# Optimization experiments

Measured on AMD Instinct MI355X. Metric: run time of the kernel, lower is better.

Reference implementation:

```python
import jax, jax.numpy as jnp
import numpy as np

B, I, C, H, W = 8, 16, 256, 64, 64  # batch, instances, channels(=in=out), spatial


def setup_inputs() -> dict:
    key = jax.random.key(0)
    ks = jax.random.split(key, 8)
    x = jax.random.normal(ks[0], (B, C, H, W), dtype=jnp.float32)
    masks = jax.random.uniform(ks[1], (B, I, H, W), dtype=jnp.float32)
    # conv_feat: 1x1 conv C->C  -> weight [C_out, C_in]
    Wf = jax.random.normal(ks[2], (C, C), dtype=jnp.float32) * 0.02
    bf = jax.random.normal(ks[3], (C,), dtype=jnp.float32) * 0.02
    # conv_mask: grouped 1x1 conv, groups=I, each 1 -> C channels -> weight [I, C]
    Wm = jax.random.normal(ks[4], (I, C), dtype=jnp.float32) * 0.02
    bm = jax.random.normal(ks[5], (I, C), dtype=jnp.float32) * 0.02
    # conv_out: 1x1 conv C->C
    Wo = jax.random.normal(ks[6], (C, C), dtype=jnp.float32) * 0.02
    bo = jax.random.normal(ks[7], (C,), dtype=jnp.float32) * 0.02
    gamma = jnp.float32(0.5)  # torch init is 0.0; use nonzero so baseline is nontrivial
    return {"x": x, "masks": masks, "Wf": Wf, "bf": bf, "Wm": Wm, "bm": bm,
            "Wo": Wo, "bo": bo, "gamma": gamma}


def reference(x, masks, Wf, bf, Wm, bm, Wo, bo, gamma):
    b, i, h, w = masks.shape
    c = Wf.shape[0]
    # conv_feat: 1x1 conv == per-pixel matmul
    feat = jnp.einsum('bchw,oc->bohw', x, Wf) + bf[:, None, None]  # [B,C,H,W]
    # grouped 1x1 conv_mask: instance i channel -> C channels
    mc = (masks[:, :, None, :, :] * Wm[None, :, :, None, None]
          + bm[None, :, :, None, None])                              # [B,I,C,H,W]
    # softmax over (C*H*W) per instance, as in masks.view(B, I, -1)
    mc = jax.nn.softmax(mc.reshape(b, i, -1), axis=-1).reshape(b, i, c, h, w)
    # loop sum_i conv_out(feat * mask_i)  ==  conv_out_W @ (feat * sum_i mask_i) + I*bias
    msum = mc.sum(axis=1)                                            # [B,C,H,W]
    out = jnp.einsum('bchw,oc->bohw', feat * msum, Wo) + (i * bo)[:, None, None]
    return gamma * out + x
```

## Files before the change

kernel.cpp:

```cpp
#include <hip/hip_runtime.h>


#define NB 8
#define NI 16
#define NC 256
#define HWSZ 4096
#define PT 32

typedef __attribute__((ext_vector_type(8))) short short8;
typedef __attribute__((ext_vector_type(4))) short short4v;
typedef __attribute__((ext_vector_type(4))) float f32x4;

static __device__ inline short f2bf(float f) {
    unsigned u = __builtin_bit_cast(unsigned, f);
    u += 0x7fffu + ((u >> 16) & 1u);
    return (short)(u >> 16);
}
static __device__ inline float bf2f(short h) {
    unsigned u = ((unsigned)(unsigned short)h) << 16;
    return __builtin_bit_cast(float, u);
}


__global__ __launch_bounds__(256)
void setup_kernel(const float* __restrict__ masks, const float* __restrict__ Wm,
                  const float* __restrict__ bm, const float* __restrict__ Wf,
                  const float* __restrict__ Wo, short* __restrict__ AhatF,
                  short* __restrict__ WfF, short* __restrict__ WoF) {
    const int blk = blockIdx.x, t = threadIdx.x;
    if (blk >= NB * NI) {
        const int pid = (blk - NB * NI) * 256 + t;
        const float* src = (pid < 8192) ? Wf : Wo;
        short* dst       = (pid < 8192) ? WfF : WoF;
        const int r  = pid & 8191;
        const int l  = r & 63;
        const int ot = (r >> 6) & 3;
        const int ks = (r >> 8) & 7;
        const int w  = (r >> 11) & 3;
        const int o  = w * 64 + ot * 16 + (l & 15);
        const int c0 = ks * 32 + (l >> 4) * 8;
        float4 v0 = *(const float4*)(src + o * NC + c0);
        float4 v1 = *(const float4*)(src + o * NC + c0 + 4);
        short8 p = { f2bf(v0.x), f2bf(v0.y), f2bf(v0.z), f2bf(v0.w),
                     f2bf(v1.x), f2bf(v1.y), f2bf(v1.z), f2bf(v1.w) };
        *(short8*)(dst + r * 8) = p;
        return;
    }
    const int bi = blk;
    const int b  = bi >> 4;
    const int i  = bi & (NI - 1);
    const float* m = masks + (size_t)bi * HWSZ;

    float s1 = 0.f, s2 = 0.f, s3 = 0.f, s4 = 0.f, s5 = 0.f, s6 = 0.f;
    for (int e = t; e < HWSZ; e += 256) {
        float v = m[e];
        float v2 = v * v, v3 = v2 * v;
        s1 += v; s2 += v2; s3 += v3;
        s4 += v2 * v2; s5 += v2 * v3; s6 += v3 * v3;
    }
    __shared__ float red[7][4];
    float sv[6] = { s1, s2, s3, s4, s5, s6 };
#pragma unroll
    for (int k = 0; k < 6; ++k) {
        float v = sv[k];
#pragma unroll
        for (int off = 32; off > 0; off >>= 1) v += __shfl_down(v, off, 64);
        if ((t & 63) == 0) red[k][t >> 6] = v;
    }
    __syncthreads();
    const float S1 = red[0][0] + red[0][1] + red[0][2] + red[0][3];
    const float S2 = red[1][0] + red[1][1] + red[1][2] + red[1][3];
    const float S3 = red[2][0] + red[2][1] + red[2][2] + red[2][3];
    const float S4 = red[3][0] + red[3][1] + red[3][2] + red[3][3];
    const float S5 = red[4][0] + red[4][1] + red[4][2] + red[4][3];
    const float S6 = red[5][0] + red[5][1] + red[5][2] + red[5][3];

    const int c = t;
    const float w  = Wm[i * NC + c];
    const float eb = __expf(bm[i * NC + c]);
    const float poly = (float)HWSZ
        + w * (S1 + w * (0.5f * S2 + w * ((1.f / 6.f) * S3
        + w * ((1.f / 24.f) * S4 + w * ((1.f / 120.f) * S5
        + w * ((1.f / 720.f) * S6))))));
    float v = eb * poly;
#pragma unroll
    for (int off = 32; off > 0; off >>= 1) v += __shfl_down(v, off, 64);
    if ((t & 63) == 0) red[6][t >> 6] = v;
    __syncthreads();
    const float Z = red[6][0] + red[6][1] + red[6][2] + red[6][3];
    const float a = eb / Z;
    const int wv   = c >> 6;
    const int ot   = (c >> 4) & 3;
    const int ln15 = c & 15;
    const int ks   = i >> 3;
    const int qq   = (i >> 1) & 3;
    const int l    = qq * 16 + ln15;
    const int js   = (i & 1) * 4;
    short4v av = { f2bf(a), f2bf(a * w), f2bf(a * w * w * 0.5f),
                   f2bf(a * w * w * w * (1.f / 6.f)) };
    *(short4v*)(AhatF + ((((b * 4 + wv) * 2 + ks) * 4 + ot) * 64 + l) * 8 + js) = av;
}

__global__ __launch_bounds__(256, 4)
void main_kernel(const float* __restrict__ x, const float* __restrict__ masks,
                 const float* __restrict__ bf_, const float* __restrict__ bo,
                 const float* __restrict__ gamma_p,
                 const short* __restrict__ WfF, const short* __restrict__ WoF,
                 const short* __restrict__ AhatF, float* __restrict__ out) {
    const int blk  = blockIdx.x;
    const int b    = blk >> 7;
    const int hw0  = (blk & 127) << 5;
    const int t    = threadIdx.x;
    const int lane = t & 63;
    const int ln15 = lane & 15;
    const int q    = lane >> 4;
    const int w    = t >> 6;
    const int wo0  = w << 6;

    __shared__ __align__(16) short smem[10752];
    short* sA = smem;
    short* sM = smem + 8448;

    const float* xbase = x + ((size_t)b * NC) * HWSZ + hw0;

    const int cth = t >> 3;
    const int qf  = t & 7;
    float4 xr[8];
#pragma unroll
    for (int it = 0; it < 8; ++it)
        xr[it] = *(const float4*)(xbase + (size_t)(it * 32 + cth) * HWSZ + qf * 4);

    {
        const int i  = t >> 4;
        const int p2 = (t & 15) * 2;
        const float* mp = masks + ((size_t)(b * NI + i)) * HWSZ + hw0 + p2;
        float m0 = mp[0], m1 = mp[1];
        float m0s = m0 * m0, m1s = m1 * m1;
        short4v v0 = { (short)0x3F80, f2bf(m0), f2bf(m0s), f2bf(m0s * m0) };
        short4v v1 = { (short)0x3F80, f2bf(m1), f2bf(m1s), f2bf(m1s * m1) };
        *(short4v*)(sM + p2 * 72 + i * 4) = v0;
        *(short4v*)(sM + (p2 + 1) * 72 + i * 4) = v1;
    }

#pragma unroll
    for (int it = 0; it < 8; ++it) {
        const int c = it * 32 + cth;
        sA[(qf * 4 + 0) * 264 + c] = f2bf(xr[it].x);
        sA[(qf * 4 + 1) * 264 + c] = f2bf(xr[it].y);
        sA[(qf * 4 + 2) * 264 + c] = f2bf(xr[it].z);
        sA[(qf * 4 + 3) * 264 + c] = f2bf(xr[it].w);
    }
    __syncthreads();

    f32x4 feat[4][2];
#pragma unroll
    for (int ot = 0; ot < 4; ++ot)
#pragma unroll
        for (int pt = 0; pt < 2; ++pt) feat[ot][pt] = (f32x4)0.f;
#pragma unroll 4
    for (int ks = 0; ks < 8; ++ks) {
        short8 af[4], bfr[2];
#pragma unroll
        for (int ot = 0; ot < 4; ++ot)
            af[ot] = *(const short8*)(WfF + (((w * 8 + ks) * 4 + ot) * 64 + lane) * 8);
#pragma unroll
        for (int pt = 0; pt < 2; ++pt)
            bfr[pt] = *(const short8*)(sA + (pt * 16 + ln15) * 264 + ks * 32 + q * 8);
#pragma unroll
        for (int ot = 0; ot < 4; ++ot)
#pragma unroll
            for (int pt = 0; pt < 2; ++pt)
                feat[ot][pt] = __builtin_amdgcn_mfma_f32_16x16x32_bf16(
                    af[ot], bfr[pt], feat[ot][pt], 0, 0, 0);
    }
    __syncthreads();

    {
        short8 mfr[2][2];
#pragma unroll
        for (int ks = 0; ks < 2; ++ks)
#pragma unroll
            for (int pt = 0; pt < 2; ++pt)
                mfr[ks][pt] = *(const short8*)(sM + (pt * 16 + ln15) * 72
                                               + ks * 32 + q * 8);
        const short* Ab = AhatF + (size_t)b * 2048 * 8;
#pragma unroll
        for (int ot = 0; ot < 4; ++ot) {
            f32x4 macc[2];
            macc[0] = (f32x4)0.f; macc[1] = (f32x4)0.f;
#pragma unroll
            for (int ks = 0; ks < 2; ++ks) {
                short8 a0 = *(const short8*)(Ab + (((w * 2 + ks) * 4 + ot) * 64
                                                   + lane) * 8);
#pragma unroll
                for (int pt = 0; pt < 2; ++pt)
                    macc[pt] = __builtin_amdgcn_mfma_f32_16x16x32_bf16(
                        a0, mfr[ks][pt], macc[pt], 0, 0, 0);
            }
            float4 bv = *(const float4*)(bf_ + wo0 + ot * 16 + q * 4);
            float b4[4] = { bv.x, bv.y, bv.z, bv.w };
#pragma unroll
            for (int pt = 0; pt < 2; ++pt) {
                short4v zz;
#pragma unroll
                for (int r = 0; r < 4; ++r)
                    zz[r] = f2bf((feat[ot][pt][r] + b4[r]) * macc[pt][r]);
                *(short4v*)(sA + (pt * 16 + ln15) * 264 + wo0 + ot * 16 + q * 4) = zz;
            }
        }
    }
    __syncthreads();

    f32x4 oacc[4][2];
#pragma unroll
    for (int ot = 0; ot < 4; ++ot)
#pragma unroll
        for (int pt = 0; pt < 2; ++pt) oacc[ot][pt] = (f32x4)0.f;
#pragma unroll 4
    for (int ks = 0; ks < 8; ++ks) {
        short8 af[4], bfr[2];
#pragma unroll
        for (int ot = 0; ot < 4; ++ot)
            af[ot] = *(const short8*)(WoF + (((w * 8 + ks) * 4 + ot) * 64 + lane) * 8);
#pragma unroll
        for (int pt = 0; pt < 2; ++pt)
            bfr[pt] = *(const short8*)(sA + (pt * 16 + ln15) * 264 + ks * 32 + q * 8);
#pragma unroll
        for (int ot = 0; ot < 4; ++ot)
#pragma unroll
            for (int pt = 0; pt < 2; ++pt)
                oacc[ot][pt] = __builtin_amdgcn_mfma_f32_16x16x32_bf16(
                    af[ot], bfr[pt], oacc[ot][pt], 0, 0, 0);
    }
    __syncthreads();

#pragma unroll
    for (int ot = 0; ot < 4; ++ot)
#pragma unroll
        for (int pt = 0; pt < 2; ++pt)
#pragma unroll
            for (int r = 0; r < 4; ++r)
                smem[(wo0 + ot * 16 + q * 4 + r) * 36 + pt * 16 + ln15] =
                    f2bf(oacc[ot][pt][r]);
    __syncthreads();

    const float g = gamma_p[0];
    float* ob = out + ((size_t)b * NC) * HWSZ + hw0;
#pragma unroll
    for (int it = 0; it < 8; ++it) {
        const int o = it * 32 + cth;
        short4v zb = *(const short4v*)(smem + o * 36 + qf * 4);
        float bov = 16.0f * bo[o];
        float4 r;
        r.x = g * (bf2f(zb[0]) + bov) + xr[it].x;
        r.y = g * (bf2f(zb[1]) + bov) + xr[it].y;
        r.z = g * (bf2f(zb[2]) + bov) + xr[it].z;
        r.w = g * (bf2f(zb[3]) + bov) + xr[it].w;
        *(float4*)(ob + (size_t)o * HWSZ + qf * 4) = r;
    }
}

extern "C" void kernel_launch(void* const* d_in, const int* in_sizes, int n_in,
                              void* d_out, int out_size, void* d_ws, size_t ws_size,
                              hipStream_t stream) {
    const float* x     = (const float*)d_in[0];
    const float* masks = (const float*)d_in[1];
    const float* Wf    = (const float*)d_in[2];
    const float* bf    = (const float*)d_in[3];
    const float* Wm    = (const float*)d_in[4];
    const float* bm    = (const float*)d_in[5];
    const float* Wo    = (const float*)d_in[6];
    const float* bo    = (const float*)d_in[7];
    const float* gamma = (const float*)d_in[8];
    float* out = (float*)d_out;

    short* ws    = (short*)d_ws;
    short* WfF   = ws;
    short* WoF   = WfF + 65536;
    short* AhatF = WoF + 65536;

    hipLaunchKernelGGL(setup_kernel, dim3(NB * NI + 64), dim3(256), 0, stream,
                       masks, Wm, bm, Wf, Wo, AhatF, WfF, WoF);
    hipLaunchKernelGGL(main_kernel, dim3(NB * (HWSZ / PT)), dim3(256), 0, stream,
                       x, masks, bf, bo, gamma, WfF, WoF, AhatF, out);
}
```

Before: 118.0 us.

## Process two pixel tiles per block with prefetch of the second tile

Each block now handles 64 pixels as two 32-pixel tiles. The x and mask loads for the second tile are issued before the first tile's compute, so global memory latency overlaps with MFMA work. The grid shrinks from 1024 to 512 blocks, shared memory roughly doubles, and launch bounds drop to 2 blocks per CU. The extra registers held for the prefetched tile and the fewer waves in flight may reduce latency hiding elsewhere.

```diff
diff --git a/kernel.cpp b/kernel.cpp
--- a/kernel.cpp
+++ b/kernel.cpp
@@ -5,7 +5,6 @@
 #define NI 16
 #define NC 256
 #define HWSZ 4096
-#define PT 32
 
 typedef __attribute__((ext_vector_type(8))) short short8;
 typedef __attribute__((ext_vector_type(4))) short short4v;
@@ -101,163 +100,207 @@
     *(short4v*)(AhatF + ((((b * 4 + wv) * 2 + ks) * 4 + ot) * 64 + l) * 8 + js) = av;
 }
 
-__global__ __launch_bounds__(256, 4)
+static __device__ __forceinline__
+void tile_compute(short* sbuf, const float4* xr,
+                  const short* __restrict__ WfF, const short* __restrict__ WoF,
+                  const short* __restrict__ Ab, const float* __restrict__ bf_,
+                  const float* bov, float g, float* __restrict__ ob,
+                  int lane, int ln15, int q, int w, int wo0, int cth, int qf) {
+    short* sA = sbuf;
+    short* sM = sbuf + 8448;
+
+    f32x4 feat[4][2];
+#pragma unroll
+    for (int ot = 0; ot < 4; ++ot)
+#pragma unroll
+        for (int pt = 0; pt < 2; ++pt) feat[ot][pt] = (f32x4)0.f;
+#pragma unroll 4
+    for (int ks = 0; ks < 8; ++ks) {
+        short8 af[4], bfr[2];
+#pragma unroll
+        for (int ot = 0; ot < 4; ++ot)
+            af[ot] = *(const short8*)(WfF + (((w * 8 + ks) * 4 + ot) * 64 + lane) * 8);
+#pragma unroll
+        for (int pt = 0; pt < 2; ++pt)
+            bfr[pt] = *(const short8*)(sA + (pt * 16 + ln15) * 264 + ks * 32 + q * 8);
+#pragma unroll
+        for (int ot = 0; ot < 4; ++ot)
+#pragma unroll
+            for (int pt = 0; pt < 2; ++pt)
+                feat[ot][pt] = __builtin_amdgcn_mfma_f32_16x16x32_bf16(
+                    af[ot], bfr[pt], feat[ot][pt], 0, 0, 0);
+    }
+    __syncthreads();
+
+    {
+        short8 mfr[2][2];
+#pragma unroll
+        for (int ks = 0; ks < 2; ++ks)
+#pragma unroll
+            for (int pt = 0; pt < 2; ++pt)
+                mfr[ks][pt] = *(const short8*)(sM + (pt * 16 + ln15) * 72
+                                               + ks * 32 + q * 8);
+#pragma unroll
+        for (int ot = 0; ot < 4; ++ot) {
+            f32x4 macc[2];
+            macc[0] = (f32x4)0.f; macc[1] = (f32x4)0.f;
+#pragma unroll
+            for (int ks = 0; ks < 2; ++ks) {
+                short8 a0 = *(const short8*)(Ab + (((w * 2 + ks) * 4 + ot) * 64
+                                                   + lane) * 8);
+#pragma unroll
+                for (int pt = 0; pt < 2; ++pt)
+                    macc[pt] = __builtin_amdgcn_mfma_f32_16x16x32_bf16(
+                        a0, mfr[ks][pt], macc[pt], 0, 0, 0);
+            }
+            float4 bv = *(const float4*)(bf_ + wo0 + ot * 16 + q * 4);
+            float b4[4] = { bv.x, bv.y, bv.z, bv.w };
+#pragma unroll
+            for (int pt = 0; pt < 2; ++pt) {
+                short4v zz;
+#pragma unroll
+                for (int r = 0; r < 4; ++r)
+                    zz[r] = f2bf((feat[ot][pt][r] + b4[r]) * macc[pt][r]);
+                *(short4v*)(sA + (pt * 16 + ln15) * 264 + wo0 + ot * 16 + q * 4) = zz;
+            }
+        }
+    }
+    __syncthreads();
+
+    f32x4 oacc[4][2];
+#pragma unroll
+    for (int ot = 0; ot < 4; ++ot)
+#pragma unroll
+        for (int pt = 0; pt < 2; ++pt) oacc[ot][pt] = (f32x4)0.f;
+#pragma unroll 4
+    for (int ks = 0; ks < 8; ++ks) {
+        short8 af[4], bfr[2];
+#pragma unroll
+        for (int ot = 0; ot < 4; ++ot)
+            af[ot] = *(const short8*)(WoF + (((w * 8 + ks) * 4 + ot) * 64 + lane) * 8);
+#pragma unroll
+        for (int pt = 0; pt < 2; ++pt)
+            bfr[pt] = *(const short8*)(sA + (pt * 16 + ln15) * 264 + ks * 32 + q * 8);
+#pragma unroll
+        for (int ot = 0; ot < 4; ++ot)
+#pragma unroll
+            for (int pt = 0; pt < 2; ++pt)
+                oacc[ot][pt] = __builtin_amdgcn_mfma_f32_16x16x32_bf16(
+                    af[ot], bfr[pt], oacc[ot][pt], 0, 0, 0);
+    }
+    __syncthreads();
+
+#pragma unroll
+    for (int ot = 0; ot < 4; ++ot)
+#pragma unroll
+        for (int pt = 0; pt < 2; ++pt)
+#pragma unroll
+            for (int r = 0; r < 4; ++r)
+                sbuf[(wo0 + ot * 16 + q * 4 + r) * 36 + pt * 16 + ln15] =
+                    f2bf(oacc[ot][pt][r]);
+    __syncthreads();
+
+#pragma unroll
+    for (int it = 0; it < 8; ++it) {
+        const int o = it * 32 + cth;
+        short4v zb = *(const short4v*)(sbuf + o * 36 + qf * 4);
+        float4 r;
+        r.x = g * (bf2f(zb[0]) + bov[it]) + xr[it].x;
+        r.y = g * (bf2f(zb[1]) + bov[it]) + xr[it].y;
+        r.z = g * (bf2f(zb[2]) + bov[it]) + xr[it].z;
+        r.w = g * (bf2f(zb[3]) + bov[it]) + xr[it].w;
+        *(float4*)(ob + (size_t)o * HWSZ + qf * 4) = r;
+    }
+}
+
+__global__ __launch_bounds__(256, 2)
 void main_kernel(const float* __restrict__ x, const float* __restrict__ masks,
                  const float* __restrict__ bf_, const float* __restrict__ bo,
                  const float* __restrict__ gamma_p,
                  const short* __restrict__ WfF, const short* __restrict__ WoF,
                  const short* __restrict__ AhatF, float* __restrict__ out) {
     const int blk  = blockIdx.x;
-    const int b    = blk >> 7;
-    const int hw0  = (blk & 127) << 5;
+    const int b    = blk >> 6;
+    const int hwp  = (blk & 63) << 6;
     const int t    = threadIdx.x;
     const int lane = t & 63;
     const int ln15 = lane & 15;
     const int q    = lane >> 4;
     const int w    = t >> 6;
     const int wo0  = w << 6;
-
-    __shared__ __align__(16) short smem[10752];
-    short* sA = smem;
-    short* sM = smem + 8448;
-
-    const float* xbase = x + ((size_t)b * NC) * HWSZ + hw0;
-
-    const int cth = t >> 3;
-    const int qf  = t & 7;
-    float4 xr[8];
+    const int cth  = t >> 3;
+    const int qf   = t & 7;
+
+    __shared__ __align__(16) short smem[19200];
+
+    const float* xb0 = x + ((size_t)b * NC) * HWSZ + hwp;
+    const float* xb1 = xb0 + 32;
+    const float* mrow = masks + ((size_t)b * NI) * HWSZ + hwp;
+    const int mi  = t >> 4;
+    const int mp2 = (t & 15) * 2;
+
+    float mk0a = mrow[(size_t)mi * HWSZ + mp2];
+    float mk0b = mrow[(size_t)mi * HWSZ + mp2 + 1];
+    float4 xr0[8];
 #pragma unroll
     for (int it = 0; it < 8; ++it)
-        xr[it] = *(const float4*)(xbase + (size_t)(it * 32 + cth) * HWSZ + qf * 4);
-
+        xr0[it] = *(const float4*)(xb0 + (size_t)(it * 32 + cth) * HWSZ + qf * 4);
     {
-        const int i  = t >> 4;
-        const int p2 = (t & 15) * 2;
-        const float* mp = masks + ((size_t)(b * NI + i)) * HWSZ + hw0 + p2;
-        float m0 = mp[0], m1 = mp[1];
-        float m0s = m0 * m0, m1s = m1 * m1;
-        short4v v0 = { (short)0x3F80, f2bf(m0), f2bf(m0s), f2bf(m0s * m0) };
-        short4v v1 = { (short)0x3F80, f2bf(m1), f2bf(m1s), f2bf(m1s * m1) };
-        *(short4v*)(sM + p2 * 72 + i * 4) = v0;
-        *(short4v*)(sM + (p2 + 1) * 72 + i * 4) = v1;
-    }
-
+        float m0s = mk0a * mk0a, m1s = mk0b * mk0b;
+        short4v v0 = { (short)0x3F80, f2bf(mk0a), f2bf(m0s), f2bf(m0s * mk0a) };
+        short4v v1 = { (short)0x3F80, f2bf(mk0b), f2bf(m1s), f2bf(m1s * mk0b) };
+        *(short4v*)(smem + 8448 + mp2 * 72 + mi * 4) = v0;
+        *(short4v*)(smem + 8448 + (mp2 + 1) * 72 + mi * 4) = v1;
+    }
 #pragma unroll
     for (int it = 0; it < 8; ++it) {
         const int c = it * 32 + cth;
-        sA[(qf * 4 + 0) * 264 + c] = f2bf(xr[it].x);
-        sA[(qf * 4 + 1) * 264 + c] = f2bf(xr[it].y);
-        sA[(qf * 4 + 2) * 264 + c] = f2bf(xr[it].z);
-        sA[(qf * 4 + 3) * 264 + c] = f2bf(xr[it].w);
-    }
-    __syncthreads();
-
-    f32x4 feat[4][2];
-#pragma unroll
-    for (int ot = 0; ot < 4; ++ot)
-#pragma unroll
-        for (int pt = 0; pt < 2; ++pt) feat[ot][pt] = (f32x4)0.f;
-#pragma unroll 4
-    for (int ks = 0; ks < 8; ++ks) {
-        short8 af[4], bfr[2];
-#pragma unroll
-        for (int ot = 0; ot < 4; ++ot)
-            af[ot] = *(const short8*)(WfF + (((w * 8 + ks) * 4 + ot) * 64 + lane) * 8);
-#pragma unroll
-        for (int pt = 0; pt < 2; ++pt)
-            bfr[pt] = *(const short8*)(sA + (pt * 16 + ln15) * 264 + ks * 32 + q * 8);
-#pragma unroll
-        for (int ot = 0; ot < 4; ++ot)
-#pragma unroll
-            for (int pt = 0; pt < 2; ++pt)
-                feat[ot][pt] = __builtin_amdgcn_mfma_f32_16x16x32_bf16(
-                    af[ot], bfr[pt], feat[ot][pt], 0, 0, 0);
-    }
-    __syncthreads();
-
+        smem[(qf * 4 + 0) * 264 + c] = f2bf(xr0[it].x);
+        smem[(qf * 4 + 1) * 264 + c] = f2bf(xr0[it].y);
+        smem[(qf * 4 + 2) * 264 + c] = f2bf(xr0[it].z);
+        smem[(qf * 4 + 3) * 264 + c] = f2bf(xr0[it].w);
+    }
+    __syncthreads();
+
+    float mk1a = mrow[(size_t)mi * HWSZ + 32 + mp2];
+    float mk1b = mrow[(size_t)mi * HWSZ + 32 + mp2 + 1];
+    float4 xr1[8];
+#pragma unroll
+    for (int it = 0; it < 8; ++it)
+        xr1[it] = *(const float4*)(xb1 + (size_t)(it * 32 + cth) * HWSZ + qf * 4);
     {
-        short8 mfr[2][2];
-#pragma unroll
-        for (int ks = 0; ks < 2; ++ks)
-#pragma unroll
-            for (int pt = 0; pt < 2; ++pt)
-                mfr[ks][pt] = *(const short8*)(sM + (pt * 16 + ln15) * 72
-                                               + ks * 32 + q * 8);
-        const short* Ab = AhatF + (size_t)b * 2048 * 8;
-#pragma unroll
-        for (int ot = 0; ot < 4; ++ot) {
-            f32x4 macc[2];
-            macc[0] = (f32x4)0.f; macc[1] = (f32x4)0.f;
-#pragma unroll
-            for (int ks = 0; ks < 2; ++ks) {
-                short8 a0 = *(const short8*)(Ab + (((w * 2 + ks) * 4 + ot) * 64
-                                                   + lane) * 8);
-#pragma unroll
-                for (int pt = 0; pt < 2; ++pt)
-                    macc[pt] = __builtin_amdgcn_mfma_f32_16x16x32_bf16(
-                        a0, mfr[ks][pt], macc[pt], 0, 0, 0);
-            }
-            float4 bv = *(const float4*)(bf_ + wo0 + ot * 16 + q * 4);
-            float b4[4] = { bv.x, bv.y, bv.z, bv.w };
-#pragma unroll
-            for (int pt = 0; pt < 2; ++pt) {
-                short4v zz;
-#pragma unroll
-                for (int r = 0; r < 4; ++r)
-                    zz[r] = f2bf((feat[ot][pt][r] + b4[r]) * macc[pt][r]);
-                *(short4v*)(sA + (pt * 16 + ln15) * 264 + wo0 + ot * 16 + q * 4) = zz;
-            }
-        }
-    }
-    __syncthreads();
-
-    f32x4 oacc[4][2];
-#pragma unroll
-    for (int ot = 0; ot < 4; ++ot)
-#pragma unroll
-        for (int pt = 0; pt < 2; ++pt) oacc[ot][pt] = (f32x4)0.f;
-#pragma unroll 4
-    for (int ks = 0; ks < 8; ++ks) {
-        short8 af[4], bfr[2];
-#pragma unroll
-        for (int ot = 0; ot < 4; ++ot)
-            af[ot] = *(const short8*)(WoF + (((w * 8 + ks) * 4 + ot) * 64 + lane) * 8);
-#pragma unroll
-        for (int pt = 0; pt < 2; ++pt)
-            bfr[pt] = *(const short8*)(sA + (pt * 16 + ln15) * 264 + ks * 32 + q * 8);
-#pragma unroll
-        for (int ot = 0; ot < 4; ++ot)
-#pragma unroll
-            for (int pt = 0; pt < 2; ++pt)
-                oacc[ot][pt] = __builtin_amdgcn_mfma_f32_16x16x32_bf16(
-                    af[ot], bfr[pt], oacc[ot][pt], 0, 0, 0);
-    }
-    __syncthreads();
-
-#pragma unroll
-    for (int ot = 0; ot < 4; ++ot)
-#pragma unroll
-        for (int pt = 0; pt < 2; ++pt)
-#pragma unroll
-            for (int r = 0; r < 4; ++r)
-                smem[(wo0 + ot * 16 + q * 4 + r) * 36 + pt * 16 + ln15] =
-                    f2bf(oacc[ot][pt][r]);
-    __syncthreads();
+        float m0s = mk1a * mk1a, m1s = mk1b * mk1b;
+        short4v v0 = { (short)0x3F80, f2bf(mk1a), f2bf(m0s), f2bf(m0s * mk1a) };
+        short4v v1 = { (short)0x3F80, f2bf(mk1b), f2bf(m1s), f2bf(m1s * mk1b) };
+        *(short4v*)(smem + 9600 + 8448 + mp2 * 72 + mi * 4) = v0;
+        *(short4v*)(smem + 9600 + 8448 + (mp2 + 1) * 72 + mi * 4) = v1;
+    }
+    __builtin_amdgcn_sched_barrier(0);
 
     const float g = gamma_p[0];
-    float* ob = out + ((size_t)b * NC) * HWSZ + hw0;
+    float bov[8];
+#pragma unroll
+    for (int it = 0; it < 8; ++it) bov[it] = 16.0f * bo[it * 32 + cth];
+
+    const short* Ab = AhatF + (size_t)b * 2048 * 8;
+    float* ob0 = out + ((size_t)b * NC) * HWSZ + hwp;
+
+    tile_compute(smem, xr0, WfF, WoF, Ab, bf_, bov, g, ob0,
+                 lane, ln15, q, w, wo0, cth, qf);
+
 #pragma unroll
     for (int it = 0; it < 8; ++it) {
-        const int o = it * 32 + cth;
-        short4v zb = *(const short4v*)(smem + o * 36 + qf * 4);
-        float bov = 16.0f * bo[o];
-        float4 r;
-        r.x = g * (bf2f(zb[0]) + bov) + xr[it].x;
-        r.y = g * (bf2f(zb[1]) + bov) + xr[it].y;
-        r.z = g * (bf2f(zb[2]) + bov) + xr[it].z;
-        r.w = g * (bf2f(zb[3]) + bov) + xr[it].w;
-        *(float4*)(ob + (size_t)o * HWSZ + qf * 4) = r;
-    }
+        const int c = it * 32 + cth;
+        short* sA1 = smem + 9600;
+        sA1[(qf * 4 + 0) * 264 + c] = f2bf(xr1[it].x);
+        sA1[(qf * 4 + 1) * 264 + c] = f2bf(xr1[it].y);
+        sA1[(qf * 4 + 2) * 264 + c] = f2bf(xr1[it].z);
+        sA1[(qf * 4 + 3) * 264 + c] = f2bf(xr1[it].w);
+    }
+    __syncthreads();
+
+    tile_compute(smem + 9600, xr1, WfF, WoF, Ab, bf_, bov, g, ob0 + 32,
+                 lane, ln15, q, w, wo0, cth, qf);
 }
 
 extern "C" void kernel_launch(void* const* d_in, const int* in_sizes, int n_in,
@@ -281,6 +324,6 @@
 
     hipLaunchKernelGGL(setup_kernel, dim3(NB * NI + 64), dim3(256), 0, stream,
                        masks, Wm, bm, Wf, Wo, AhatF, WfF, WoF);
-    hipLaunchKernelGGL(main_kernel, dim3(NB * (HWSZ / PT)), dim3(256), 0, stream,
+    hipLaunchKernelGGL(main_kernel, dim3(512), dim3(256), 0, stream,
                        x, masks, bf, bo, gamma, WfF, WoF, AhatF, out);
 }
```

Result: slower. 121.6 us (+3.0%).
